# Kernel optimization log

Measured on AMD Instinct MI355X. Metric: run time of the kernel, lower is better.

Reference implementation:

```python
import jax, jax.numpy as jnp
import numpy as np

VOCAB = 100000
EMB = 128
N = 1048576
EPS = 1e-12  # torch f.normalize default eps


def setup_inputs() -> dict:
    key = jax.random.key(0)
    k1, k2, k3, k4, k5, k6, k7, k8 = jax.random.split(key, 8)
    bound_enc = 1.0 / np.sqrt(VOCAB)
    bound_dec = 1.0 / np.sqrt(EMB)
    return {
        "x": jax.random.randint(k1, (N,), 0, VOCAB),
        "y": jax.random.randint(k2, (N,), 0, VOCAB),
        # encoder Linear(input_size, embedding_size): weight [EMB, VOCAB], bias [EMB]
        "W": jax.random.uniform(k3, (EMB, VOCAB), jnp.float32, -bound_enc, bound_enc),
        "b": jax.random.uniform(k4, (EMB,), jnp.float32, -bound_enc, bound_enc),
        # decoder heads Linear(EMB, 1)
        "w1": jax.random.uniform(k5, (1, EMB), jnp.float32, -bound_dec, bound_dec),
        "b1": jax.random.uniform(k6, (1,), jnp.float32, -bound_dec, bound_dec),
        "w2": jax.random.uniform(k7, (1, EMB), jnp.float32, -bound_dec, bound_dec),
        "b2": jax.random.uniform(k8, (1,), jnp.float32, -bound_dec, bound_dec),
    }


def _encode(idx, W, b):
    # one_hot(idx) @ W.T + b  ==  W.T[idx] + b  (row gather)
    e = jnp.take(W.T, idx, axis=0) + b  # [N, EMB]
    n = jnp.linalg.norm(e, axis=-1, keepdims=True)
    return e / jnp.maximum(n, EPS)  # torch F.normalize(p=2, dim=-1)


def reference(x, y, W, b, w1, b1, w2, b2):
    ex = _encode(x, W, b)  # [N, EMB]
    ey = _encode(y, W, b)  # [N, EMB]
    h = ex * ey            # [N, EMB]
    out1 = jax.nn.sigmoid(h @ w1.T + b1)  # [N, 1]
    out2 = jax.nn.sigmoid(h @ w2.T + b2)  # [N, 1]
    return (out1, out2)
```

## Files before the change

kernel.cpp:

```cpp
#include <hip/hip_runtime.h>
#include <hip/hip_bf16.h>
#include <hip/hip_fp16.h>

#define VOCAB 100000
#define EMB 128
#define EPS 1e-12f

typedef __attribute__((ext_vector_type(4))) unsigned int uint4_t;
typedef __attribute__((ext_vector_type(2))) float float2_t;

__device__ __forceinline__ float sigmoidf_(float z) {
    return 1.f / (1.f + __expf(-z));
}

__global__ __launch_bounds__(256) void build_table_fp8_kernel(
    const float* __restrict__ W, const float* __restrict__ b,
    unsigned int* __restrict__ nt) {
    int v = blockIdx.x * 256 + threadIdx.x;
    if (v >= VOCAB) return;

    float ss = 0.f;
    unsigned int stash[64];
#pragma unroll
    for (int j = 0; j < 64; ++j) {
        float e0 = W[(size_t)(2 * j) * VOCAB + v] + b[2 * j];
        float e1 = W[(size_t)(2 * j + 1) * VOCAB + v] + b[2 * j + 1];
        ss = fmaf(e0, e0, ss);
        ss = fmaf(e1, e1, ss);
        stash[j] = __builtin_bit_cast(unsigned int, __floats2half2_rn(e0, e1));
    }
    float inv = 1.0f / fmaxf(sqrtf(ss), EPS);

    unsigned int packed[32];
#pragma unroll
    for (int j = 0; j < 32; ++j) {
        __half2 h0 = __builtin_bit_cast(__half2, stash[2 * j]);
        __half2 h1 = __builtin_bit_cast(__half2, stash[2 * j + 1]);
        float e0 = __low2float(h0) * inv, e1 = __high2float(h0) * inv;
        float e2 = __low2float(h1) * inv, e3 = __high2float(h1) * inv;
        unsigned int u = __builtin_amdgcn_cvt_pk_fp8_f32(e0, e1, 0u, false);
        u = __builtin_amdgcn_cvt_pk_fp8_f32(e2, e3, u, true);
        packed[j] = u;
    }
    uint4_t* row = (uint4_t*)(nt + (size_t)v * 32);
#pragma unroll
    for (int q = 0; q < 8; ++q) {
        uint4_t pk;
        pk[0] = packed[4 * q + 0];
        pk[1] = packed[4 * q + 1];
        pk[2] = packed[4 * q + 2];
        pk[3] = packed[4 * q + 3];
        row[q] = pk;
    }
}

__global__ __launch_bounds__(256) void fused_gather_fp8_kernel(
    const int* __restrict__ x, const int* __restrict__ y,
    const unsigned int* __restrict__ nt,
    const float* __restrict__ w1, const float* __restrict__ b1p,
    const float* __restrict__ w2, const float* __restrict__ b2p,
    float* __restrict__ out, int n) {
    const int tid = threadIdx.x;
    const int l = tid & 7;
    const int group = blockIdx.x * 32 + (tid >> 3);
    const int ng = gridDim.x * 32;

    float w1f[16], w2f[16];
#pragma unroll
    for (int k = 0; k < 16; ++k) {
        w1f[k] = w1[l * 16 + k];
        w2f[k] = w2[l * 16 + k];
    }
    const float bb1 = *b1p, bb2 = *b2p;

    const uint4_t* base = (const uint4_t*)nt;

    int i0 = group, i1 = group + ng;
    int c0 = (i0 < n) ? i0 : 0;
    int c1 = (i1 < n) ? i1 : 0;
    int ix0 = x[c0], iy0 = y[c0];
    int ix1 = x[c1], iy1 = y[c1];

    while (i0 < n) {
        uint4_t vx0 = base[(size_t)ix0 * 8 + l];
        uint4_t vy0 = base[(size_t)iy0 * 8 + l];
        uint4_t vx1 = base[(size_t)ix1 * 8 + l];
        uint4_t vy1 = base[(size_t)iy1 * 8 + l];

        const int i0n = i0 + 2 * ng, i1n = i1 + 2 * ng;
        const int c0n = (i0n < n) ? i0n : 0;
        const int c1n = (i1n < n) ? i1n : 0;
        const int ix0n = x[c0n], iy0n = y[c0n];
        const int ix1n = x[c1n], iy1n = y[c1n];

        float d1a = 0.f, d2a = 0.f, d1b = 0.f, d2b = 0.f;
#pragma unroll
        for (int q = 0; q < 4; ++q) {
            float2_t xlo = __builtin_amdgcn_cvt_pk_f32_fp8(vx0[q], false);
            float2_t xhi = __builtin_amdgcn_cvt_pk_f32_fp8(vx0[q], true);
            float2_t ylo = __builtin_amdgcn_cvt_pk_f32_fp8(vy0[q], false);
            float2_t yhi = __builtin_amdgcn_cvt_pk_f32_fp8(vy0[q], true);
            float h0 = xlo[0] * ylo[0];
            float h1 = xlo[1] * ylo[1];
            float h2 = xhi[0] * yhi[0];
            float h3 = xhi[1] * yhi[1];
            d1a = fmaf(h0, w1f[4 * q + 0], d1a);
            d2a = fmaf(h0, w2f[4 * q + 0], d2a);
            d1a = fmaf(h1, w1f[4 * q + 1], d1a);
            d2a = fmaf(h1, w2f[4 * q + 1], d2a);
            d1a = fmaf(h2, w1f[4 * q + 2], d1a);
            d2a = fmaf(h2, w2f[4 * q + 2], d2a);
            d1a = fmaf(h3, w1f[4 * q + 3], d1a);
            d2a = fmaf(h3, w2f[4 * q + 3], d2a);
        }
#pragma unroll
        for (int q = 0; q < 4; ++q) {
            float2_t xlo = __builtin_amdgcn_cvt_pk_f32_fp8(vx1[q], false);
            float2_t xhi = __builtin_amdgcn_cvt_pk_f32_fp8(vx1[q], true);
            float2_t ylo = __builtin_amdgcn_cvt_pk_f32_fp8(vy1[q], false);
            float2_t yhi = __builtin_amdgcn_cvt_pk_f32_fp8(vy1[q], true);
            float h0 = xlo[0] * ylo[0];
            float h1 = xlo[1] * ylo[1];
            float h2 = xhi[0] * yhi[0];
            float h3 = xhi[1] * yhi[1];
            d1b = fmaf(h0, w1f[4 * q + 0], d1b);
            d2b = fmaf(h0, w2f[4 * q + 0], d2b);
            d1b = fmaf(h1, w1f[4 * q + 1], d1b);
            d2b = fmaf(h1, w2f[4 * q + 1], d2b);
            d1b = fmaf(h2, w1f[4 * q + 2], d1b);
            d2b = fmaf(h2, w2f[4 * q + 2], d2b);
            d1b = fmaf(h3, w1f[4 * q + 3], d1b);
            d2b = fmaf(h3, w2f[4 * q + 3], d2b);
        }
#pragma unroll
        for (int off = 1; off <= 4; off <<= 1) {
            d1a += __shfl_xor(d1a, off, 64);
            d2a += __shfl_xor(d2a, off, 64);
            d1b += __shfl_xor(d1b, off, 64);
            d2b += __shfl_xor(d2b, off, 64);
        }
        if (l == 0)                    out[i0]     = sigmoidf_(d1a + bb1);
        else if (l == 1)               out[n + i0] = sigmoidf_(d2a + bb2);
        else if (l == 2 && i1 < n)     out[i1]     = sigmoidf_(d1b + bb1);
        else if (l == 3 && i1 < n)     out[n + i1] = sigmoidf_(d2b + bb2);

        i0 = i0n; i1 = i1n;
        ix0 = ix0n; iy0 = iy0n; ix1 = ix1n; iy1 = iy1n;
    }
}

__global__ __launch_bounds__(256) void fused_direct_kernel(
    const int* __restrict__ x, const int* __restrict__ y,
    const float* __restrict__ W, const float* __restrict__ b,
    const float* __restrict__ w1, const float* __restrict__ b1p,
    const float* __restrict__ w2, const float* __restrict__ b2p,
    float* __restrict__ out, int n) {
    const int tid = threadIdx.x;
    const int lane16 = tid & 15;

    float bl[8], w1f[8], w2f[8];
#pragma unroll
    for (int k = 0; k < 8; ++k) {
        bl[k]  = b[lane16 * 8 + k];
        w1f[k] = w1[lane16 * 8 + k];
        w2f[k] = w2[lane16 * 8 + k];
    }
    const float bb1 = *b1p, bb2 = *b2p;

    const int group   = blockIdx.x * (blockDim.x >> 4) + (tid >> 4);
    const int ngroups = gridDim.x * (blockDim.x >> 4);

    for (int i = group; i < n; i += ngroups) {
        const int ix = x[i];
        const int iy = y[i];
        float ex[8], ey[8];
        float ssx = 0.f, ssy = 0.f;
#pragma unroll
        for (int k = 0; k < 8; ++k) {
            int j = lane16 * 8 + k;
            ex[k] = W[(size_t)j * VOCAB + ix] + bl[k];
            ey[k] = W[(size_t)j * VOCAB + iy] + bl[k];
            ssx = fmaf(ex[k], ex[k], ssx);
            ssy = fmaf(ey[k], ey[k], ssy);
        }
#pragma unroll
        for (int off = 8; off >= 1; off >>= 1) {
            ssx += __shfl_xor(ssx, off, 64);
            ssy += __shfl_xor(ssy, off, 64);
        }
        float invx = 1.0f / fmaxf(sqrtf(ssx), EPS);
        float invy = 1.0f / fmaxf(sqrtf(ssy), EPS);

        float d1 = 0.f, d2 = 0.f;
#pragma unroll
        for (int k = 0; k < 8; ++k) {
            float h = (ex[k] * invx) * (ey[k] * invy);
            d1 = fmaf(h, w1f[k], d1);
            d2 = fmaf(h, w2f[k], d2);
        }
#pragma unroll
        for (int off = 8; off >= 1; off >>= 1) {
            d1 += __shfl_xor(d1, off, 64);
            d2 += __shfl_xor(d2, off, 64);
        }
        if (lane16 == 0) {
            out[i]     = sigmoidf_(d1 + bb1);
            out[n + i] = sigmoidf_(d2 + bb2);
        }
    }
}

extern "C" void kernel_launch(void* const* d_in, const int* in_sizes, int n_in,
                              void* d_out, int out_size, void* d_ws, size_t ws_size,
                              hipStream_t stream) {
    const int*   x  = (const int*)d_in[0];
    const int*   y  = (const int*)d_in[1];
    const float* W  = (const float*)d_in[2];
    const float* b  = (const float*)d_in[3];
    const float* w1 = (const float*)d_in[4];
    const float* b1 = (const float*)d_in[5];
    const float* w2 = (const float*)d_in[6];
    const float* b2 = (const float*)d_in[7];
    float* out = (float*)d_out;
    const int n = in_sizes[0];

    const size_t table_bytes = (size_t)VOCAB * EMB;

    if (ws_size >= table_bytes && n > 0) {
        unsigned int* nt = (unsigned int*)d_ws;
        build_table_fp8_kernel<<<(VOCAB + 255) / 256, 256, 0, stream>>>(W, b, nt);
        int blocks = 2048;
        if (n < 2048 * 32) blocks = (n + 31) / 32;
        if (blocks < 1) blocks = 1;
        fused_gather_fp8_kernel<<<blocks, 256, 0, stream>>>(x, y, nt, w1, b1, w2, b2, out, n);
    } else if (n > 0) {
        int ngroups = (n + 15) / 16;
        int blocks  = (ngroups + 15) / 16;
        if (blocks > 8192) blocks = 8192;
        if (blocks < 1) blocks = 1;
        fused_direct_kernel<<<blocks, 256, 0, stream>>>(x, y, W, b, w1, b1, w2, b2, out, n);
    }
}
```

Before: 54.95 us.

## Quantize normalized embedding table to FP4 with per-row scale for gather

Adds an FP4 (e2m1) table path: each vocab row is normalized, scaled by its max, and packed into 64 bytes plus a per-row float scale. The gather kernel then reads 8 bytes per lane instead of 16 and decodes with the hardware scaled FP4 convert instruction, applying the combined scale after the dot product. The aim is to halve the random-gather traffic, and the table now fits more easily in cache. The cost is a large loss of precision (4-bit values) that may break accuracy tolerance, plus an extra scalar scale load per index.

```diff
diff --git a/kernel.cpp b/kernel.cpp
--- a/kernel.cpp
+++ b/kernel.cpp
@@ -7,10 +7,164 @@
 #define EPS 1e-12f
 
 typedef __attribute__((ext_vector_type(4))) unsigned int uint4_t;
+typedef __attribute__((ext_vector_type(2))) unsigned int uint2_t;
 typedef __attribute__((ext_vector_type(2))) float float2_t;
 
 __device__ __forceinline__ float sigmoidf_(float z) {
     return 1.f / (1.f + __expf(-z));
+}
+
+#if __has_builtin(__builtin_amdgcn_cvt_scalef32_pk_f32_fp4)
+#define HAVE_FP4 1
+#else
+#define HAVE_FP4 0
+#endif
+
+#if HAVE_FP4
+
+__device__ __forceinline__ unsigned int quant_e2m1(float q) {
+    float a = fabsf(q);
+    unsigned int c = (a > 0.25f) + (a > 0.75f) + (a > 1.25f) + (a > 1.75f) +
+                     (a > 2.5f) + (a > 3.5f) + (a > 5.0f);
+    return c | ((q < 0.f) ? 8u : 0u);
+}
+
+__global__ __launch_bounds__(256) void build_table_fp4_kernel(
+    const float* __restrict__ W, const float* __restrict__ b,
+    unsigned int* __restrict__ nt4, float* __restrict__ scl) {
+    const int tid = threadIdx.x;
+    const int col = blockIdx.x * 64 + (tid >> 2);
+    const int sub = tid & 3;
+    if (col >= VOCAB) return;
+
+    float ss = 0.f, mmax = 0.f;
+    unsigned int stash[16];
+#pragma unroll
+    for (int t = 0; t < 16; ++t) {
+        int j = sub * 32 + 2 * t;
+        float e0 = W[(size_t)j * VOCAB + col] + b[j];
+        float e1 = W[(size_t)(j + 1) * VOCAB + col] + b[j + 1];
+        ss = fmaf(e0, e0, ss);
+        ss = fmaf(e1, e1, ss);
+        mmax = fmaxf(mmax, fmaxf(fabsf(e0), fabsf(e1)));
+        stash[t] = __builtin_bit_cast(unsigned int, __floats2half2_rn(e0, e1));
+    }
+    ss += __shfl_xor(ss, 1, 64);
+    ss += __shfl_xor(ss, 2, 64);
+    mmax = fmaxf(mmax, __shfl_xor(mmax, 1, 64));
+    mmax = fmaxf(mmax, __shfl_xor(mmax, 2, 64));
+
+    float inv = 1.0f / fmaxf(sqrtf(ss), EPS);
+    float nmax = fmaxf(mmax * inv, 1e-30f);
+    float S = nmax * (1.0f / 6.0f);
+    float invS = 6.0f / nmax;
+
+    unsigned int words[4] = {0u, 0u, 0u, 0u};
+#pragma unroll
+    for (int t = 0; t < 16; ++t) {
+        __half2 h2 = __builtin_bit_cast(__half2, stash[t]);
+        float q0 = __low2float(h2) * inv * invS;
+        float q1 = __high2float(h2) * inv * invS;
+        unsigned int c0 = quant_e2m1(q0);
+        unsigned int c1 = quant_e2m1(q1);
+        words[t >> 2] |= (c0 << (8 * (t & 3))) | (c1 << (8 * (t & 3) + 4));
+    }
+    uint4_t pk;
+    pk[0] = words[0]; pk[1] = words[1]; pk[2] = words[2]; pk[3] = words[3];
+    *(uint4_t*)(nt4 + (size_t)col * 16 + sub * 4) = pk;
+    if (sub == 0) scl[col] = S;
+}
+
+#define CVT4(u, s) __builtin_amdgcn_cvt_scalef32_pk_f32_fp4((u), 1.0f, (s))
+
+__global__ __launch_bounds__(256) void fused_gather_fp4_kernel(
+    const int* __restrict__ x, const int* __restrict__ y,
+    const unsigned int* __restrict__ nt4, const float* __restrict__ scl,
+    const float* __restrict__ w1, const float* __restrict__ b1p,
+    const float* __restrict__ w2, const float* __restrict__ b2p,
+    float* __restrict__ out, int n) {
+    const int tid = threadIdx.x;
+    const int l = tid & 7;
+    const int group = blockIdx.x * 32 + (tid >> 3);
+    const int ng = gridDim.x * 32;
+
+    float2_t w1v[8], w2v[8];
+    const float2_t* w1p = (const float2_t*)w1;
+    const float2_t* w2p = (const float2_t*)w2;
+#pragma unroll
+    for (int q = 0; q < 8; ++q) {
+        w1v[q] = w1p[l * 8 + q];
+        w2v[q] = w2p[l * 8 + q];
+    }
+    const float bb1 = *b1p, bb2 = *b2p;
+
+    const uint2_t* base = (const uint2_t*)nt4;
+
+    int i0 = group, i1 = group + ng;
+    int c0 = (i0 < n) ? i0 : 0;
+    int c1 = (i1 < n) ? i1 : 0;
+    int ix0 = x[c0], iy0 = y[c0];
+    int ix1 = x[c1], iy1 = y[c1];
+
+    while (i0 < n) {
+        uint2_t rx0 = base[(size_t)ix0 * 8 + l];
+        uint2_t ry0 = base[(size_t)iy0 * 8 + l];
+        uint2_t rx1 = base[(size_t)ix1 * 8 + l];
+        uint2_t ry1 = base[(size_t)iy1 * 8 + l];
+        float sx0 = scl[ix0], sy0 = scl[iy0];
+        float sx1 = scl[ix1], sy1 = scl[iy1];
+
+        const int i0n = i0 + 2 * ng, i1n = i1 + 2 * ng;
+        const int c0n = (i0n < n) ? i0n : 0;
+        const int c1n = (i1n < n) ? i1n : 0;
+        const int ix0n = x[c0n], iy0n = y[c0n];
+        const int ix1n = x[c1n], iy1n = y[c1n];
+
+        float2_t a1 = {0.f, 0.f}, a2 = {0.f, 0.f};
+        float2_t e1v = {0.f, 0.f}, e2v = {0.f, 0.f};
+        {
+            float2_t h;
+            h = CVT4(rx0[0], 0) * CVT4(ry0[0], 0); a1 += h * w1v[0]; a2 += h * w2v[0];
+            h = CVT4(rx0[0], 1) * CVT4(ry0[0], 1); a1 += h * w1v[1]; a2 += h * w2v[1];
+            h = CVT4(rx0[0], 2) * CVT4(ry0[0], 2); a1 += h * w1v[2]; a2 += h * w2v[2];
+            h = CVT4(rx0[0], 3) * CVT4(ry0[0], 3); a1 += h * w1v[3]; a2 += h * w2v[3];
+            h = CVT4(rx0[1], 0) * CVT4(ry0[1], 0); a1 += h * w1v[4]; a2 += h * w2v[4];
+            h = CVT4(rx0[1], 1) * CVT4(ry0[1], 1); a1 += h * w1v[5]; a2 += h * w2v[5];
+            h = CVT4(rx0[1], 2) * CVT4(ry0[1], 2); a1 += h * w1v[6]; a2 += h * w2v[6];
+            h = CVT4(rx0[1], 3) * CVT4(ry0[1], 3); a1 += h * w1v[7]; a2 += h * w2v[7];
+            h = CVT4(rx1[0], 0) * CVT4(ry1[0], 0); e1v += h * w1v[0]; e2v += h * w2v[0];
+            h = CVT4(rx1[0], 1) * CVT4(ry1[0], 1); e1v += h * w1v[1]; e2v += h * w2v[1];
+            h = CVT4(rx1[0], 2) * CVT4(ry1[0], 2); e1v += h * w1v[2]; e2v += h * w2v[2];
+            h = CVT4(rx1[0], 3) * CVT4(ry1[0], 3); e1v += h * w1v[3]; e2v += h * w2v[3];
+            h = CVT4(rx1[1], 0) * CVT4(ry1[1], 0); e1v += h * w1v[4]; e2v += h * w2v[4];
+            h = CVT4(rx1[1], 1) * CVT4(ry1[1], 1); e1v += h * w1v[5]; e2v += h * w2v[5];
+            h = CVT4(rx1[1], 2) * CVT4(ry1[1], 2); e1v += h * w1v[6]; e2v += h * w2v[6];
+            h = CVT4(rx1[1], 3) * CVT4(ry1[1], 3); e1v += h * w1v[7]; e2v += h * w2v[7];
+        }
+        float d1a = a1[0] + a1[1], d2a = a2[0] + a2[1];
+        float d1b = e1v[0] + e1v[1], d2b = e2v[0] + e2v[1];
+#pragma unroll
+        for (int off = 1; off <= 4; off <<= 1) {
+            d1a += __shfl_xor(d1a, off, 64);
+            d2a += __shfl_xor(d2a, off, 64);
+            d1b += __shfl_xor(d1b, off, 64);
+            d2b += __shfl_xor(d2b, off, 64);
+        }
+        const float sa = sx0 * sy0, sb = sx1 * sy1;
+        if (l == 0)                out[i0]     = sigmoidf_(fmaf(d1a, sa, bb1));
+        else if (l == 1)           out[n + i0] = sigmoidf_(fmaf(d2a, sa, bb2));
+        else if (l == 2 && i1 < n) out[i1]     = sigmoidf_(fmaf(d1b, sb, bb1));
+        else if (l == 3 && i1 < n) out[n + i1] = sigmoidf_(fmaf(d2b, sb, bb2));
+
+        i0 = i0n; i1 = i1n;
+        ix0 = ix0n; iy0 = iy0n; ix1 = ix1n; iy1 = iy1n;
+    }
+}
+#endif
+
+__device__ __forceinline__ unsigned int f2bf_(float f) {
+    __hip_bfloat16 h = __float2bfloat16(f);
+    return (unsigned int)__builtin_bit_cast(unsigned short, h);
 }
 
 __global__ __launch_bounds__(256) void build_table_fp8_kernel(
@@ -72,7 +226,6 @@
         w2f[k] = w2[l * 16 + k];
     }
     const float bb1 = *b1p, bb2 = *b2p;
-
     const uint4_t* base = (const uint4_t*)nt;
 
     int i0 = group, i1 = group + ng;
@@ -139,10 +292,10 @@
             d1b += __shfl_xor(d1b, off, 64);
             d2b += __shfl_xor(d2b, off, 64);
         }
-        if (l == 0)                    out[i0]     = sigmoidf_(d1a + bb1);
-        else if (l == 1)               out[n + i0] = sigmoidf_(d2a + bb2);
-        else if (l == 2 && i1 < n)     out[i1]     = sigmoidf_(d1b + bb1);
-        else if (l == 3 && i1 < n)     out[n + i1] = sigmoidf_(d2b + bb2);
+        if (l == 0)                out[i0]     = sigmoidf_(d1a + bb1);
+        else if (l == 1)           out[n + i0] = sigmoidf_(d2a + bb2);
+        else if (l == 2 && i1 < n) out[i1]     = sigmoidf_(d1b + bb1);
+        else if (l == 3 && i1 < n) out[n + i1] = sigmoidf_(d2b + bb2);
 
         i0 = i0n; i1 = i1n;
         ix0 = ix0n; iy0 = iy0n; ix1 = ix1n; iy1 = iy1n;
@@ -223,17 +376,30 @@
     const float* b2 = (const float*)d_in[7];
     float* out = (float*)d_out;
     const int n = in_sizes[0];
-
-    const size_t table_bytes = (size_t)VOCAB * EMB;
-
-    if (ws_size >= table_bytes && n > 0) {
+    if (n <= 0) return;
+
+#if HAVE_FP4
+    const size_t fp4_bytes = (size_t)VOCAB * 64 + (size_t)VOCAB * 4;
+    if (ws_size >= fp4_bytes) {
+        unsigned int* nt4 = (unsigned int*)d_ws;
+        float* scl = (float*)((char*)d_ws + (size_t)VOCAB * 64);
+        build_table_fp4_kernel<<<(VOCAB + 63) / 64, 256, 0, stream>>>(W, b, nt4, scl);
+        int blocks = 2048;
+        if (n < 2048 * 32) blocks = (n + 31) / 32;
+        if (blocks < 1) blocks = 1;
+        fused_gather_fp4_kernel<<<blocks, 256, 0, stream>>>(x, y, nt4, scl, w1, b1, w2, b2, out, n);
+        return;
+    }
+#endif
+    const size_t fp8_bytes = (size_t)VOCAB * EMB;
+    if (ws_size >= fp8_bytes) {
         unsigned int* nt = (unsigned int*)d_ws;
         build_table_fp8_kernel<<<(VOCAB + 255) / 256, 256, 0, stream>>>(W, b, nt);
         int blocks = 2048;
         if (n < 2048 * 32) blocks = (n + 31) / 32;
         if (blocks < 1) blocks = 1;
         fused_gather_fp8_kernel<<<blocks, 256, 0, stream>>>(x, y, nt, w1, b1, w2, b2, out, n);
-    } else if (n > 0) {
+    } else {
         int ngroups = (n + 15) / 16;
         int blocks  = (ngroups + 15) / 16;
         if (blocks > 8192) blocks = 8192;
```

Result: no change. 54.55 us (-0.7%).
